# Optimization experiments

Hardware: AMD Instinct MI355X
Metric: run time of the kernel (lower is better)

## Reference

```python
import jax, jax.numpy as jnp
import numpy as np

B, L, D = 4, 1024, 1024
H = 16
DH = D // H  # 64
CACHE_LEN = 1024


def setup_inputs() -> dict:
    key = jax.random.key(0)
    ks = jax.random.split(key, 12)
    s = 1.0 / np.sqrt(D)
    return {
        "query": jax.random.normal(ks[0], (B, L, D), jnp.float32),
        "key": jax.random.normal(ks[1], (B, L, D), jnp.float32),
        "value": jax.random.normal(ks[2], (B, L, D), jnp.float32),
        "cache": jax.random.normal(ks[3], (B, H, CACHE_LEN, 2 * DH), jnp.float32),
        "Wq": jax.random.normal(ks[4], (D, D), jnp.float32) * s,
        "bq": jnp.zeros((D,), jnp.float32),
        "Wk": jax.random.normal(ks[5], (D, D), jnp.float32) * s,
        "bk": jnp.zeros((D,), jnp.float32),
        "Wv": jax.random.normal(ks[6], (D, D), jnp.float32) * s,
        "bv": jnp.zeros((D,), jnp.float32),
        "Wo": jax.random.normal(ks[7], (D, D), jnp.float32) * s,
        "bo": jnp.zeros((D,), jnp.float32),
    }


def _split_heads(x):
    # (B, L, D) -> (B, H, L, DH)
    b, l, _ = x.shape
    return x.reshape(b, l, H, DH).transpose(0, 2, 1, 3)


def reference(query, key, value, cache, Wq, bq, Wk, bk, Wv, bv, Wo, bo):
    q = _split_heads(query @ Wq.T + bq)   # (B,H,Lq,DH)
    k = _split_heads(key @ Wk.T + bk)     # (B,H,Lk,DH)
    v = _split_heads(value @ Wv.T + bv)   # (B,H,Lk,DH)

    # KV-cache concat along sequence dim
    key_cache, value_cache = jnp.split(cache, 2, axis=-1)
    k = jnp.concatenate([key_cache, k], axis=2)   # (B,H,Lc+Lk,DH)
    v = jnp.concatenate([value_cache, v], axis=2)
    new_cache = jnp.concatenate([k, v], axis=-1)  # (B,H,Lc+Lk,2*DH)

    scores = jnp.einsum("bhqd,bhkd->bhqk", q, k) / jnp.sqrt(jnp.float32(DH))
    attn = jax.nn.softmax(scores, axis=-1)        # unmasked path (mask sentinel empty)
    out = jnp.einsum("bhqk,bhkd->bhqd", attn, v)  # (B,H,Lq,DH)
    out = out.transpose(0, 2, 1, 3).reshape(query.shape[0], -1, H * DH)
    out = out @ Wo.T + bo                         # (B,Lq,D)
    return (out, new_cache)
```

## Files before the change

kernel.cpp:

```cpp
#include <hip/hip_runtime.h>
#include <hip/hip_bf16.h>
#include <stdint.h>

constexpr int Hh = 16, Ll = 1024, Dd = 1024, DHh = 64, CL = 1024, TKV = 2048;
constexpr size_t OUT_ELEMS = 4ull * 1024 * 1024;
constexpr float LOG2E = 1.44269504088896340736f;

typedef __attribute__((ext_vector_type(8))) short short8;
typedef __attribute__((ext_vector_type(4))) float floatx4;

#define MFMA16(a, b, c) __builtin_amdgcn_mfma_f32_16x16x32_bf16(a, b, c, 0, 0, 0)

__device__ __forceinline__ float fexp2(float x) {
#if __has_builtin(__builtin_amdgcn_exp2f)
    return __builtin_amdgcn_exp2f(x);
#else
    float r;
    asm("v_exp_f32 %0, %1" : "=v"(r) : "v"(x));
    return r;
#endif
}

__device__ __forceinline__ short bfs(float x) {
    union { __hip_bfloat16 h; short s; } u;
    u.h = __float2bfloat16(x);
    return u.s;
}

__device__ __forceinline__ short8 cvt8(const float* p) {
    float4 a = *(const float4*)p;
    float4 b = *(const float4*)(p + 4);
    short8 r;
    r[0] = bfs(a.x); r[1] = bfs(a.y); r[2] = bfs(a.z); r[3] = bfs(a.w);
    r[4] = bfs(b.x); r[5] = bfs(b.y); r[6] = bfs(b.z); r[7] = bfs(b.w);
    return r;
}

__device__ __forceinline__ void gload_lds16(const __hip_bfloat16* g, __hip_bfloat16* l) {
    __builtin_amdgcn_global_load_lds((const __attribute__((address_space(1))) void*)g,
                                     (__attribute__((address_space(3))) void*)l, 16, 0, 0);
}

__device__ __forceinline__ int vswz(int d) { return ((d >> 3) ^ d) & 7; }

__global__ __launch_bounds__(256) void prep_kernel(
    const float* __restrict__ cache, const float* __restrict__ Wq,
    const float* __restrict__ Wk, const float* __restrict__ Wv,
    const float* __restrict__ Wo, float* __restrict__ outc,
    __hip_bfloat16* __restrict__ Wb, __hip_bfloat16* __restrict__ kbf,
    __hip_bfloat16* __restrict__ vbf) {
    if (blockIdx.x < 4096) {
        int c = blockIdx.x * 256 + threadIdx.x;
        int bh  = c >> 14;
        int rem = c & 16383;
        int t = rem >> 4, part = rem & 15;
        const float* s = cache + (size_t)c * 8;
        float* d = outc + OUT_ELEMS + (size_t)bh * 262144 + (size_t)rem * 8;
        *(float4*)d       = *(const float4*)s;
        *(float4*)(d + 4) = *(const float4*)(s + 4);
        short8 bv = cvt8(s);
        if (part < 8) {
            *(short8*)&kbf[(size_t)bh * 131072 + (size_t)t * 64 +
                           ((part ^ (t & 7)) << 3)] = bv;
        } else {
            int d0 = (part - 8) * 8;
#pragma unroll
            for (int e = 0; e < 8; e++) {
                int dd = d0 + e;
                ((short*)vbf)[((size_t)(bh * 16 + (t >> 7)) * 64 + dd) * 128 +
                              ((t & 127) ^ (vswz(dd) << 3))] = bv[e];
            }
        }
    } else {
        int c = (blockIdx.x - 4096) * 256 + threadIdx.x;
        int wsel = c >> 17;
        int within = c & 131071;
        const float* src = (wsel == 0) ? Wq : (wsel == 1) ? Wk : (wsel == 2) ? Wv : Wo;
        *(short8*)(Wb + (size_t)c * 8) = cvt8(src + (size_t)within * 8);
    }
}

__global__ __launch_bounds__(256) void gemm_qkv(
    const float* __restrict__ Aq, const float* __restrict__ Ak,
    const float* __restrict__ Av, const __hip_bfloat16* __restrict__ Wb,
    const float* __restrict__ bq, const float* __restrict__ bk,
    const float* __restrict__ bv, __hip_bfloat16* __restrict__ qws,
    float* __restrict__ outc, __hip_bfloat16* __restrict__ kbf,
    __hip_bfloat16* __restrict__ vbf) {
    constexpr int K = 1024, BK = 64;
    __shared__ alignas(16) __hip_bfloat16 As[64 * BK];
    __shared__ alignas(16) __hip_bfloat16 Bs[128 * BK];

    const int mode = blockIdx.z;
    const float* A = (mode == 0) ? Aq : (mode == 1) ? Ak : Av;
    const float* bias = (mode == 0) ? bq : (mode == 1) ? bk : bv;
    const __hip_bfloat16* W = Wb + ((size_t)mode << 20);

    const int tid = threadIdx.x;
    const int w = tid >> 6, lane = tid & 63;
    const int g = lane >> 4, lr = lane & 15;
    const int tm = blockIdx.x * 64, tn = blockIdx.y * 128;
    const int wr = (w >> 1) * 32, wc = (w & 1) * 64;

    floatx4 acc[2][4] = {};

    for (int k0 = 0; k0 < K; k0 += BK) {
        __syncthreads();
#pragma unroll
        for (int it = 0; it < 4; it++) {
            int c0 = it * 256 + w * 64;
            int c = c0 + lane;
            int row = c >> 3, col = (c & 7) * 8;
            gload_lds16(W + (size_t)(tn + row) * K + k0 + col, &Bs[c0 * 8]);
        }
#pragma unroll
        for (int it = 0; it < 2; it++) {
            int c = it * 256 + tid;
            int row = c >> 3, col = (c & 7) * 8;
            *(short8*)&As[c * 8] = cvt8(A + (size_t)(tm + row) * K + k0 + col);
        }
        __syncthreads();
#pragma unroll
        for (int kk = 0; kk < 2; kk++) {
            short8 af[2], bf[4];
#pragma unroll
            for (int i = 0; i < 2; i++)
                af[i] = *(const short8*)&As[(wr + i * 16 + lr) * BK + kk * 32 + g * 8];
#pragma unroll
            for (int j = 0; j < 4; j++)
                bf[j] = *(const short8*)&Bs[(wc + j * 16 + lr) * BK + kk * 32 + g * 8];
#pragma unroll
            for (int i = 0; i < 2; i++)
#pragma unroll
                for (int j = 0; j < 4; j++)
                    acc[i][j] = MFMA16(af[i], bf[j], acc[i][j]);
        }
    }

#pragma unroll
    for (int j = 0; j < 4; j++) {
        int n = tn + wc + j * 16 + lr;
        float bv_ = bias[n];
#pragma unroll
        for (int i = 0; i < 2; i++) {
#pragma unroll
            for (int r = 0; r < 4; r++) {
                int m = tm + wr + i * 16 + g * 4 + r;
                float v = acc[i][j][r] + bv_;
                if (mode == 0) {
                    size_t addr = (size_t)(m >> 10) * ((size_t)Hh * Ll * DHh) +
                                  (size_t)(n >> 6) * ((size_t)Ll * DHh) +
                                  (size_t)(m & 1023) * DHh + (n & 63);
                    qws[addr] = __float2bfloat16(v * (0.125f * LOG2E));
                } else {
                    size_t bh = (size_t)((m >> 10) * Hh + (n >> 6));
                    size_t addr = OUT_ELEMS + (bh * TKV + CL + (m & 1023)) * 128 + (n & 63) +
                                  (mode == 2 ? 64 : 0);
                    outc[addr] = v;
                    int t = CL + (m & 1023);
                    int dd = n & 63;
                    __hip_bfloat16 hv = __float2bfloat16(v);
                    if (mode == 1) {
                        kbf[bh * 131072 + (size_t)t * 64 +
                            (((dd >> 3) ^ (t & 7)) << 3) + (dd & 7)] = hv;
                    } else {
                        vbf[(bh * 16 + (size_t)(t >> 7)) * 8192 + (size_t)dd * 128 +
                            ((t & 127) ^ (vswz(dd) << 3))] = hv;
                    }
                }
            }
        }
    }
}

__global__ __launch_bounds__(256) void gemm_out(
    const __hip_bfloat16* __restrict__ A, const __hip_bfloat16* __restrict__ W,
    const float* __restrict__ bias, float* __restrict__ C) {
    constexpr int K = 1024, BK = 64;
    __shared__ alignas(16) __hip_bfloat16 As[64 * BK];
    __shared__ alignas(16) __hip_bfloat16 Bs[128 * BK];

    const int tid = threadIdx.x;
    const int w = tid >> 6, lane = tid & 63;
    const int g = lane >> 4, lr = lane & 15;
    const int tm = blockIdx.x * 64, tn = blockIdx.y * 128;
    const int wr = (w >> 1) * 32, wc = (w & 1) * 64;

    floatx4 acc[2][4] = {};

    for (int k0 = 0; k0 < K; k0 += BK) {
        __syncthreads();
#pragma unroll
        for (int it = 0; it < 4; it++) {
            int c0 = it * 256 + w * 64;
            int c = c0 + lane;
            int row = c >> 3, col = (c & 7) * 8;
            gload_lds16(W + (size_t)(tn + row) * K + k0 + col, &Bs[c0 * 8]);
        }
#pragma unroll
        for (int it = 0; it < 2; it++) {
            int c0 = it * 256 + w * 64;
            int c = c0 + lane;
            int row = c >> 3, col = (c & 7) * 8;
            gload_lds16(A + (size_t)(tm + row) * K + k0 + col, &As[c0 * 8]);
        }
        __syncthreads();
#pragma unroll
        for (int kk = 0; kk < 2; kk++) {
            short8 af[2], bf[4];
#pragma unroll
            for (int i = 0; i < 2; i++)
                af[i] = *(const short8*)&As[(wr + i * 16 + lr) * BK + kk * 32 + g * 8];
#pragma unroll
            for (int j = 0; j < 4; j++)
                bf[j] = *(const short8*)&Bs[(wc + j * 16 + lr) * BK + kk * 32 + g * 8];
#pragma unroll
            for (int i = 0; i < 2; i++)
#pragma unroll
                for (int j = 0; j < 4; j++)
                    acc[i][j] = MFMA16(af[i], bf[j], acc[i][j]);
        }
    }

#pragma unroll
    for (int j = 0; j < 4; j++) {
        int n = tn + wc + j * 16 + lr;
        float bv = bias[n];
#pragma unroll
        for (int i = 0; i < 2; i++)
#pragma unroll
            for (int r = 0; r < 4; r++) {
                int m = tm + wr + i * 16 + g * 4 + r;
                C[(size_t)m * 1024 + n] = acc[i][j][r] + bv;
            }
    }
}

__global__ __launch_bounds__(512) void attn_kernel(
    const __hip_bfloat16* __restrict__ qws, const __hip_bfloat16* __restrict__ kbf,
    const __hip_bfloat16* __restrict__ vbf, __hip_bfloat16* __restrict__ ows) {
    constexpr int KVB = 128;
    __shared__ alignas(16) __hip_bfloat16 Ks[2][KVB * 64];
    __shared__ alignas(16) __hip_bfloat16 Vt[2][64 * KVB];
    __shared__ alignas(16) __hip_bfloat16 Ps[8][16 * 136];

    const int tid = threadIdx.x;
    const int w = tid >> 6, lane = tid & 63;
    const int g = lane >> 4, lr = lane & 15;
    const int bh = blockIdx.x;
    const int q0 = blockIdx.y * 128 + w * 16;

    const __hip_bfloat16* qbase = qws + (size_t)bh * Ll * DHh;
    const __hip_bfloat16* kb = kbf + (size_t)bh * 131072;
    const __hip_bfloat16* vb = vbf + (size_t)bh * 131072;

    short8 qf[2];
#pragma unroll
    for (int kk = 0; kk < 2; kk++)
        qf[kk] = *(const short8*)(qbase + (size_t)(q0 + lr) * DHh + kk * 32 + g * 8);

#define STAGE(b, tl)                                                          \
    {                                                                         \
        const __hip_bfloat16* kt = kb + (size_t)(tl) * 8192;                  \
        const __hip_bfloat16* vt = vb + (size_t)(tl) * 8192;                  \
        _Pragma("unroll")                                                     \
        for (int it = 0; it < 2; it++) {                                      \
            int c0 = it * 512 + w * 64;                                       \
            gload_lds16(kt + (size_t)(c0 + lane) * 8, &Ks[b][c0 * 8]);        \
            gload_lds16(vt + (size_t)(c0 + lane) * 8, &Vt[b][c0 * 8]);        \
        }                                                                     \
    }

    float rm[4], rl[4];
    floatx4 o[4] = {};
#pragma unroll
    for (int j = 0; j < 4; j++) { rm[j] = -3e38f; rl[j] = 0.f; }

    STAGE(0, 0);
    __syncthreads();

    int cur = 0;
    for (int tl = 0; tl < 16; ++tl) {
        if (tl < 15) STAGE(cur ^ 1, tl + 1);

        floatx4 s[8];
#pragma unroll
        for (int f = 0; f < 8; f++) {
            floatx4 z = {};
            int row = f * 16 + lr;
#pragma unroll
            for (int kk = 0; kk < 2; kk++) {
                short8 bfr = *(const short8*)
                    &Ks[cur][row * 64 + (((kk * 4 + g) ^ (row & 7)) << 3)];
                z = MFMA16(qf[kk], bfr, z);
            }
            s[f] = z;
        }

        float mt[4];
#pragma unroll
        for (int j = 0; j < 4; j++) {
            float mv = fmaxf(fmaxf(fmaxf(s[0][j], s[1][j]), fmaxf(s[2][j], s[3][j])),
                             fmaxf(fmaxf(s[4][j], s[5][j]), fmaxf(s[6][j], s[7][j])));
            mv = fmaxf(mv, __shfl_xor(mv, 1));
            mv = fmaxf(mv, __shfl_xor(mv, 2));
            mv = fmaxf(mv, __shfl_xor(mv, 4));
            mv = fmaxf(mv, __shfl_xor(mv, 8));
            mt[j] = mv;
        }
        bool ok = (mt[0] - rm[0] <= 8.f) && (mt[1] - rm[1] <= 8.f) &&
                  (mt[2] - rm[2] <= 8.f) && (mt[3] - rm[3] <= 8.f);
        if (!__all(ok)) {
#pragma unroll
            for (int j = 0; j < 4; j++) {
                float mn = fmaxf(rm[j], mt[j]);
                float corr = fexp2(rm[j] - mn);
                rm[j] = mn;
                rl[j] *= corr;
#pragma unroll
                for (int f2 = 0; f2 < 4; f2++) o[f2][j] = o[f2][j] * corr;
            }
        }
        float rs[4] = {0.f, 0.f, 0.f, 0.f};
#pragma unroll
        for (int f = 0; f < 8; f++)
#pragma unroll
            for (int j = 0; j < 4; j++) {
                float p = fexp2(s[f][j] - rm[j]);
                s[f][j] = p;
                rs[j] += p;
            }
#pragma unroll
        for (int j = 0; j < 4; j++) {
            rs[j] += __shfl_xor(rs[j], 1);
            rs[j] += __shfl_xor(rs[j], 2);
            rs[j] += __shfl_xor(rs[j], 4);
            rs[j] += __shfl_xor(rs[j], 8);
            rl[j] += rs[j];
        }

        __hip_bfloat16* pw = &Ps[w][0];
#pragma unroll
        for (int f = 0; f < 8; f++)
#pragma unroll
            for (int j = 0; j < 4; j++)
                pw[(g * 4 + j) * 136 + f * 16 + lr] = __float2bfloat16(s[f][j]);

#pragma unroll
        for (int kk = 0; kk < 4; kk++) {
            short8 pa = *(const short8*)&pw[lr * 136 + kk * 32 + g * 8];
#pragma unroll
            for (int f2 = 0; f2 < 4; f2++) {
                int d = f2 * 16 + lr;
                short8 vbr = *(const short8*)
                    &Vt[cur][d * KVB + ((kk * 32 + g * 8) ^ (vswz(d) << 3))];
                o[f2] = MFMA16(pa, vbr, o[f2]);
            }
        }

        __syncthreads();
        cur ^= 1;
    }
#undef STAGE

    const int b = bh >> 4, h = bh & 15;
#pragma unroll
    for (int j = 0; j < 4; j++) {
        float inv = 1.0f / rl[j];
        int qrow = q0 + g * 4 + j;
        size_t rb = ((size_t)b * Ll + qrow) * Dd + (size_t)h * DHh;
#pragma unroll
        for (int f2 = 0; f2 < 4; f2++)
            ows[rb + f2 * 16 + lr] = __float2bfloat16(o[f2][j] * inv);
    }
}

extern "C" void kernel_launch(void* const* d_in, const int* in_sizes, int n_in,
                              void* d_out, int out_size, void* d_ws, size_t ws_size,
                              hipStream_t stream) {
    (void)in_sizes; (void)n_in; (void)out_size; (void)ws_size;
    const float* query = (const float*)d_in[0];
    const float* key   = (const float*)d_in[1];
    const float* value = (const float*)d_in[2];
    const float* cache = (const float*)d_in[3];
    const float* Wq = (const float*)d_in[4];
    const float* bq = (const float*)d_in[5];
    const float* Wk = (const float*)d_in[6];
    const float* bk = (const float*)d_in[7];
    const float* Wv = (const float*)d_in[8];
    const float* bv = (const float*)d_in[9];
    const float* Wo = (const float*)d_in[10];
    const float* bo = (const float*)d_in[11];

    float* out = (float*)d_out;
    __hip_bfloat16* qws = (__hip_bfloat16*)d_ws;
    __hip_bfloat16* aws = qws + OUT_ELEMS;
    __hip_bfloat16* Wb  = aws + OUT_ELEMS;
    __hip_bfloat16* kbf = Wb  + OUT_ELEMS;
    __hip_bfloat16* vbf = kbf + (8ull << 20);

    dim3 bb(256);
    prep_kernel<<<dim3(6144), bb, 0, stream>>>(cache, Wq, Wk, Wv, Wo, out, Wb, kbf, vbf);

    gemm_qkv<<<dim3(64, 8, 3), bb, 0, stream>>>(query, key, value, Wb, bq, bk, bv,
                                                qws, out, kbf, vbf);

    attn_kernel<<<dim3(64, 8), dim3(512), 0, stream>>>(qws, kbf, vbf, aws);

    gemm_out<<<dim3(64, 8), bb, 0, stream>>>(aws, Wb + (3u << 20), bo, out);
}
```

Measured before the change: 191.2 us.

## Process two 16-row query tiles per wave in attention kernel

Each wave now handles 32 query rows instead of 16, so every K and V fragment read from LDS feeds two MFMAs. The grid shrinks from 512 to 256 blocks and each block covers 256 query rows, which halves the total K/V global loads and LDS reads per query. The cost is more registers for scores and accumulators, a larger P buffer in LDS, and only 256 blocks to spread across the CUs, which may lower occupancy.

```diff
diff --git a/kernel.cpp b/kernel.cpp
--- a/kernel.cpp
+++ b/kernel.cpp
@@ -242,22 +242,25 @@
     constexpr int KVB = 128;
     __shared__ alignas(16) __hip_bfloat16 Ks[2][KVB * 64];
     __shared__ alignas(16) __hip_bfloat16 Vt[2][64 * KVB];
-    __shared__ alignas(16) __hip_bfloat16 Ps[8][16 * 136];
+    __shared__ alignas(16) __hip_bfloat16 Ps[8][32 * 136];
 
     const int tid = threadIdx.x;
     const int w = tid >> 6, lane = tid & 63;
     const int g = lane >> 4, lr = lane & 15;
     const int bh = blockIdx.x;
-    const int q0 = blockIdx.y * 128 + w * 16;
+    const int q0 = blockIdx.y * 256 + w * 32;
 
     const __hip_bfloat16* qbase = qws + (size_t)bh * Ll * DHh;
     const __hip_bfloat16* kb = kbf + (size_t)bh * 131072;
     const __hip_bfloat16* vb = vbf + (size_t)bh * 131072;
 
-    short8 qf[2];
-#pragma unroll
-    for (int kk = 0; kk < 2; kk++)
-        qf[kk] = *(const short8*)(qbase + (size_t)(q0 + lr) * DHh + kk * 32 + g * 8);
+    short8 qf[2][2];
+#pragma unroll
+    for (int i = 0; i < 2; i++)
+#pragma unroll
+        for (int kk = 0; kk < 2; kk++)
+            qf[i][kk] = *(const short8*)
+                (qbase + (size_t)(q0 + i * 16 + lr) * DHh + kk * 32 + g * 8);
 
 #define STAGE(b, tl)                                                          \
     {                                                                         \
@@ -271,10 +274,12 @@
         }                                                                     \
     }
 
-    float rm[4], rl[4];
-    floatx4 o[4] = {};
-#pragma unroll
-    for (int j = 0; j < 4; j++) { rm[j] = -3e38f; rl[j] = 0.f; }
+    float rm[2][4], rl[2][4];
+    floatx4 o[2][4] = {};
+#pragma unroll
+    for (int i = 0; i < 2; i++)
+#pragma unroll
+        for (int j = 0; j < 4; j++) { rm[i][j] = -3e38f; rl[i][j] = 0.f; }
 
     STAGE(0, 0);
     __syncthreads();
@@ -283,78 +288,90 @@
     for (int tl = 0; tl < 16; ++tl) {
         if (tl < 15) STAGE(cur ^ 1, tl + 1);
 
-        floatx4 s[8];
+        floatx4 s[2][8] = {};
 #pragma unroll
         for (int f = 0; f < 8; f++) {
-            floatx4 z = {};
             int row = f * 16 + lr;
 #pragma unroll
             for (int kk = 0; kk < 2; kk++) {
                 short8 bfr = *(const short8*)
                     &Ks[cur][row * 64 + (((kk * 4 + g) ^ (row & 7)) << 3)];
-                z = MFMA16(qf[kk], bfr, z);
-            }
-            s[f] = z;
-        }
-
-        float mt[4];
-#pragma unroll
-        for (int j = 0; j < 4; j++) {
-            float mv = fmaxf(fmaxf(fmaxf(s[0][j], s[1][j]), fmaxf(s[2][j], s[3][j])),
-                             fmaxf(fmaxf(s[4][j], s[5][j]), fmaxf(s[6][j], s[7][j])));
-            mv = fmaxf(mv, __shfl_xor(mv, 1));
-            mv = fmaxf(mv, __shfl_xor(mv, 2));
-            mv = fmaxf(mv, __shfl_xor(mv, 4));
-            mv = fmaxf(mv, __shfl_xor(mv, 8));
-            mt[j] = mv;
-        }
-        bool ok = (mt[0] - rm[0] <= 8.f) && (mt[1] - rm[1] <= 8.f) &&
-                  (mt[2] - rm[2] <= 8.f) && (mt[3] - rm[3] <= 8.f);
+                s[0][f] = MFMA16(qf[0][kk], bfr, s[0][f]);
+                s[1][f] = MFMA16(qf[1][kk], bfr, s[1][f]);
+            }
+        }
+
+        bool ok = true;
+        float mt[2][4];
+#pragma unroll
+        for (int i = 0; i < 2; i++)
+#pragma unroll
+            for (int j = 0; j < 4; j++) {
+                float mv = fmaxf(
+                    fmaxf(fmaxf(s[i][0][j], s[i][1][j]), fmaxf(s[i][2][j], s[i][3][j])),
+                    fmaxf(fmaxf(s[i][4][j], s[i][5][j]), fmaxf(s[i][6][j], s[i][7][j])));
+                mv = fmaxf(mv, __shfl_xor(mv, 1));
+                mv = fmaxf(mv, __shfl_xor(mv, 2));
+                mv = fmaxf(mv, __shfl_xor(mv, 4));
+                mv = fmaxf(mv, __shfl_xor(mv, 8));
+                mt[i][j] = mv;
+                ok = ok && (mv - rm[i][j] <= 8.f);
+            }
         if (!__all(ok)) {
 #pragma unroll
+            for (int i = 0; i < 2; i++)
+#pragma unroll
+                for (int j = 0; j < 4; j++) {
+                    float mn = fmaxf(rm[i][j], mt[i][j]);
+                    float corr = fexp2(rm[i][j] - mn);
+                    rm[i][j] = mn;
+                    rl[i][j] *= corr;
+#pragma unroll
+                    for (int f2 = 0; f2 < 4; f2++) o[i][f2][j] = o[i][f2][j] * corr;
+                }
+        }
+#pragma unroll
+        for (int i = 0; i < 2; i++) {
+            float rs[4] = {0.f, 0.f, 0.f, 0.f};
+#pragma unroll
+            for (int f = 0; f < 8; f++)
+#pragma unroll
+                for (int j = 0; j < 4; j++) {
+                    float p = fexp2(s[i][f][j] - rm[i][j]);
+                    s[i][f][j] = p;
+                    rs[j] += p;
+                }
+#pragma unroll
             for (int j = 0; j < 4; j++) {
-                float mn = fmaxf(rm[j], mt[j]);
-                float corr = fexp2(rm[j] - mn);
-                rm[j] = mn;
-                rl[j] *= corr;
-#pragma unroll
-                for (int f2 = 0; f2 < 4; f2++) o[f2][j] = o[f2][j] * corr;
-            }
-        }
-        float rs[4] = {0.f, 0.f, 0.f, 0.f};
-#pragma unroll
-        for (int f = 0; f < 8; f++)
-#pragma unroll
-            for (int j = 0; j < 4; j++) {
-                float p = fexp2(s[f][j] - rm[j]);
-                s[f][j] = p;
-                rs[j] += p;
-            }
-#pragma unroll
-        for (int j = 0; j < 4; j++) {
-            rs[j] += __shfl_xor(rs[j], 1);
-            rs[j] += __shfl_xor(rs[j], 2);
-            rs[j] += __shfl_xor(rs[j], 4);
-            rs[j] += __shfl_xor(rs[j], 8);
-            rl[j] += rs[j];
+                rs[j] += __shfl_xor(rs[j], 1);
+                rs[j] += __shfl_xor(rs[j], 2);
+                rs[j] += __shfl_xor(rs[j], 4);
+                rs[j] += __shfl_xor(rs[j], 8);
+                rl[i][j] += rs[j];
+            }
         }
 
         __hip_bfloat16* pw = &Ps[w][0];
 #pragma unroll
-        for (int f = 0; f < 8; f++)
-#pragma unroll
-            for (int j = 0; j < 4; j++)
-                pw[(g * 4 + j) * 136 + f * 16 + lr] = __float2bfloat16(s[f][j]);
+        for (int i = 0; i < 2; i++)
+#pragma unroll
+            for (int f = 0; f < 8; f++)
+#pragma unroll
+                for (int j = 0; j < 4; j++)
+                    pw[(i * 16 + g * 4 + j) * 136 + f * 16 + lr] =
+                        __float2bfloat16(s[i][f][j]);
 
 #pragma unroll
         for (int kk = 0; kk < 4; kk++) {
-            short8 pa = *(const short8*)&pw[lr * 136 + kk * 32 + g * 8];
+            short8 pa0 = *(const short8*)&pw[(0 + lr) * 136 + kk * 32 + g * 8];
+            short8 pa1 = *(const short8*)&pw[(16 + lr) * 136 + kk * 32 + g * 8];
 #pragma unroll
             for (int f2 = 0; f2 < 4; f2++) {
                 int d = f2 * 16 + lr;
                 short8 vbr = *(const short8*)
                     &Vt[cur][d * KVB + ((kk * 32 + g * 8) ^ (vswz(d) << 3))];
-                o[f2] = MFMA16(pa, vbr, o[f2]);
+                o[0][f2] = MFMA16(pa0, vbr, o[0][f2]);
+                o[1][f2] = MFMA16(pa1, vbr, o[1][f2]);
             }
         }
 
@@ -365,14 +382,16 @@
 
     const int b = bh >> 4, h = bh & 15;
 #pragma unroll
-    for (int j = 0; j < 4; j++) {
-        float inv = 1.0f / rl[j];
-        int qrow = q0 + g * 4 + j;
-        size_t rb = ((size_t)b * Ll + qrow) * Dd + (size_t)h * DHh;
-#pragma unroll
-        for (int f2 = 0; f2 < 4; f2++)
-            ows[rb + f2 * 16 + lr] = __float2bfloat16(o[f2][j] * inv);
-    }
+    for (int i = 0; i < 2; i++)
+#pragma unroll
+        for (int j = 0; j < 4; j++) {
+            float inv = 1.0f / rl[i][j];
+            int qrow = q0 + i * 16 + g * 4 + j;
+            size_t rb = ((size_t)b * Ll + qrow) * Dd + (size_t)h * DHh;
+#pragma unroll
+            for (int f2 = 0; f2 < 4; f2++)
+                ows[rb + f2 * 16 + lr] = __float2bfloat16(o[i][f2][j] * inv);
+        }
 }
 
 extern "C" void kernel_launch(void* const* d_in, const int* in_sizes, int n_in,
@@ -405,7 +424,7 @@
     gemm_qkv<<<dim3(64, 8, 3), bb, 0, stream>>>(query, key, value, Wb, bq, bk, bv,
                                                 qws, out, kbf, vbf);
 
-    attn_kernel<<<dim3(64, 8), dim3(512), 0, stream>>>(qws, kbf, vbf, aws);
+    attn_kernel<<<dim3(64, 4), dim3(512), 0, stream>>>(qws, kbf, vbf, aws);
 
     gemm_out<<<dim3(64, 8), bb, 0, stream>>>(aws, Wb + (3u << 20), bo, out);
 }
```

Measured after the change: 176.7 us. -7.6%, faster.
